# Performance work log

Hardware: AMD Instinct MI355X
Metric: run time of the kernel (lower is better)

## Reference

```python
import jax, jax.numpy as jnp
import numpy as np

NUM_HEADS = 8
GEM_P = 3.0
GEM_EPS = 1e-6
L2_EPS = 1e-12


def _l2norm(x):
    n = jnp.sqrt(jnp.sum(x * x, axis=-1, keepdims=True))
    return x / jnp.maximum(n, L2_EPS)


def setup_inputs() -> dict:
    key = jax.random.key(0)
    ks = jax.random.split(key, 7)
    B, Ci, H, W = 8, 256, 40, 40
    D, N = 128, 32768
    image_feat = jax.random.normal(ks[0], (B, Ci, H, W), dtype=jnp.float32)
    cloud_feat = jax.random.normal(ks[1], (N, D), dtype=jnp.float32)
    cloud_bids = jax.random.randint(ks[2], (N,), 0, B, dtype=jnp.int32)
    W1 = jax.random.normal(ks[3], (Ci, D), dtype=jnp.float32) * (1.0 / np.sqrt(Ci))
    b1 = jnp.zeros((D,), dtype=jnp.float32)
    W2 = jax.random.normal(ks[4], (D, Ci), dtype=jnp.float32) * (1.0 / np.sqrt(D))
    b2 = jnp.zeros((Ci,), dtype=jnp.float32)
    return {"image_feat": image_feat, "cloud_feat": cloud_feat, "cloud_bids": cloud_bids,
            "W1": W1, "b1": b1, "W2": W2, "b2": b2}


def _gem(x, axis):
    # generalized-mean pooling: (mean(clamp(x,eps)^p))^(1/p)
    xp = jnp.clip(x, GEM_EPS, None) ** GEM_P
    return jnp.mean(xp, axis=axis) ** (1.0 / GEM_P)


def reference(image_feat, cloud_feat, cloud_bids, W1, b1, W2, b2):
    B, Ci, H, W = image_feat.shape
    D = W1.shape[1]
    h, dh = NUM_HEADS, D // NUM_HEADS

    # image branch: permute -> linear -> tokens
    x = jnp.einsum('bchw,cd->bhwd', image_feat, W1) + b1          # [B,H,W,D]
    tok = _l2norm(x.reshape(B, H * W, D))                          # [B,HW,D]

    # window_size=1 SA: all image tokens of a batch share coord (b,0,0,0)
    # -> full self-attention per batch window; use_proj=False -> q=k=v=feats
    q = tok.reshape(B, H * W, h, dh)
    scores = jnp.einsum('bnhd,bmhd->bhnm', q, q) * (dh ** -0.5)    # [B,h,HW,HW]
    attn = jax.nn.softmax(scores, axis=-1)
    out = jnp.einsum('bhnm,bmhd->bnhd', attn, q).reshape(B, H, W, D)

    # cloud tokens: unique voxel coords -> singleton windows -> identity attention
    cloud_out = _l2norm(cloud_feat)                                # [N,D]

    # project image tokens back to image_dim channels
    img_out = jnp.einsum('bhwd,dc->bhwc', out, W2) + b2            # [B,H,W,Ci]
    img_out = jnp.transpose(img_out, (0, 3, 1, 2))                 # [B,Ci,H,W]

    # GeM pooling
    image_gem = _gem(img_out, axis=(2, 3))                         # [B,Ci]
    cp = jnp.clip(cloud_out, GEM_EPS, None) ** GEM_P
    seg = jax.ops.segment_sum(cp, cloud_bids, num_segments=B)      # [B,D]
    cnt = jax.ops.segment_sum(jnp.ones((cloud_out.shape[0], 1), cp.dtype),
                              cloud_bids, num_segments=B)
    cloud_gem = (seg / jnp.maximum(cnt, 1.0)) ** (1.0 / GEM_P)     # [B,D]

    return (img_out, cloud_out, image_gem, cloud_gem)
```

## Files before the change

kernel.cpp:

```cpp
#include <hip/hip_runtime.h>
#include <hip/hip_bf16.h>
#include <math.h>

#define BATCH 8
#define CI    256
#define HWSZ  1600
#define DDIM  128
#define NHEAD 8
#define DH    16
#define NPTS  32768

typedef __attribute__((ext_vector_type(4))) short s16x4;
typedef __attribute__((ext_vector_type(4))) float f32x4;

#if defined(__HIP_DEVICE_COMPILE__)
  #if __has_builtin(__builtin_amdgcn_mfma_f32_16x16x16bf16_1k)
    #define MFMA16(a, b, c) __builtin_amdgcn_mfma_f32_16x16x16bf16_1k(a, b, c, 0, 0, 0)
  #elif __has_builtin(__builtin_amdgcn_mfma_f32_16x16x16_bf16)
    #define MFMA16(a, b, c) __builtin_amdgcn_mfma_f32_16x16x16_bf16(a, b, c, 0, 0, 0)
  #else
    #error "no 16x16x16 bf16 mfma builtin on this device target"
  #endif
  #if __has_builtin(__builtin_amdgcn_exp2f)
    #define EXP2(x) __builtin_amdgcn_exp2f(x)
  #else
    #define EXP2(x) exp2f(x)
  #endif
#else
  #define MFMA16(a, b, c) (c)
  #define EXP2(x) (x)
#endif

union fragu {
  s16x4 s;
  unsigned int u[2];
  uint2 u2;
};

__device__ __forceinline__ unsigned int pk_bf2(float a, float b) {
  __hip_bfloat162 h = __float22bfloat162_rn(make_float2(a, b));
  return *(unsigned int*)&h;
}
__device__ __forceinline__ float bf2f(unsigned short u) {
  return __uint_as_float(((unsigned int)u) << 16);
}

__global__ __launch_bounds__(256) void kprep(
    const float* __restrict__ W1, const float* __restrict__ W2,
    const float* __restrict__ cf, const int* __restrict__ bids,
    unsigned short* __restrict__ W1s, unsigned short* __restrict__ W2s,
    float* __restrict__ cloud_out, float* __restrict__ gaw,
    float* __restrict__ cntw) {
  __shared__ float ga[BATCH * DDIM];
  __shared__ float gc[BATCH];
  int t = threadIdx.x;
  if (blockIdx.x < 64) {
    int e = blockIdx.x * 256 + t;
    int lane = e & 63, lm = lane & 15, qd = lane >> 4;
    if (e < 8192) {
      int ks = (e >> 6) & 15, dt = e >> 10;
      const float* p = W1 + (size_t)(ks * 16 + 4 * qd) * DDIM + dt * 16 + lm;
      float f0 = p[0], f1 = p[DDIM], f2 = p[2 * DDIM], f3 = p[3 * DDIM];
      *(uint2*)&W1s[(size_t)e * 4] = make_uint2(pk_bf2(f0, f1), pk_bf2(f2, f3));
    } else {
      int e2 = e - 8192;
      int ks = (e2 >> 6) & 7, ct = e2 >> 9;
      const float* p = W2 + (size_t)(ks * 16 + 4 * qd) * CI + ct * 16 + lm;
      float f0 = p[0], f1 = p[CI], f2 = p[2 * CI], f3 = p[3 * CI];
      *(uint2*)&W2s[(size_t)e2 * 4] = make_uint2(pk_bf2(f0, f1), pk_bf2(f2, f3));
    }
    return;
  }
  int bk = blockIdx.x - 64;
  for (int i = t; i < BATCH * DDIM; i += 256) ga[i] = 0.f;
  if (t < BATCH) gc[t] = 0.f;
  __syncthreads();
  for (int half = 0; half < 2; half++) {
    int r = bk * 128 + half * 64 + (t >> 2);
    int dq = (t & 3) * 32;
    const float* row = cf + (size_t)r * DDIM + dq;
    float4 v[8];
    float ss = 0.f;
#pragma unroll
    for (int j = 0; j < 8; j++) {
      v[j] = *(const float4*)(row + j * 4);
      ss += v[j].x*v[j].x + v[j].y*v[j].y + v[j].z*v[j].z + v[j].w*v[j].w;
    }
    ss += __shfl_xor(ss, 1);
    ss += __shfl_xor(ss, 2);
    float sc = 1.f / fmaxf(sqrtf(ss), 1e-12f);
    int bid = bids[r];
    if ((t & 3) == 0) atomicAdd(&gc[bid], 1.f);
    float* orow = cloud_out + (size_t)r * DDIM + dq;
    float* gb = &ga[bid * DDIM + dq];
#pragma unroll
    for (int j = 0; j < 8; j++) {
      float4 y;
      y.x = v[j].x * sc; y.y = v[j].y * sc; y.z = v[j].z * sc; y.w = v[j].w * sc;
      *(float4*)(orow + j * 4) = y;
      float c0 = fmaxf(y.x, 1e-6f), c1 = fmaxf(y.y, 1e-6f);
      float c2 = fmaxf(y.z, 1e-6f), c3 = fmaxf(y.w, 1e-6f);
      atomicAdd(&gb[j*4+0], c0*c0*c0);
      atomicAdd(&gb[j*4+1], c1*c1*c1);
      atomicAdd(&gb[j*4+2], c2*c2*c2);
      atomicAdd(&gb[j*4+3], c3*c3*c3);
    }
  }
  __syncthreads();
  for (int i = t; i < BATCH * DDIM; i += 256) gaw[(size_t)bk * 1024 + i] = ga[i];
  if (t < BATCH) cntw[bk * 8 + t] = gc[t];
}

__global__ __launch_bounds__(256) void k1_mfma(
    const float* __restrict__ img, const unsigned short* __restrict__ W1s,
    const float* __restrict__ b1, unsigned short* __restrict__ tokh) {
  int t = threadIdx.x, lane = t & 63, w = t >> 6;
  int lm = lane & 15, qd = lane >> 4;
  int blk = blockIdx.x;
  int b = blk / 25, n0 = (blk % 25) * 64;
  int tok = n0 + w * 16 + lm;
  const float* imgb = img + (size_t)b * CI * HWSZ;
  const s16x4* W1s4 = (const s16x4*)W1s;
  float fv[16][4];
#pragma unroll
  for (int ks = 0; ks < 16; ks++) {
    const float* p = imgb + (size_t)(ks * 16 + 4 * qd) * HWSZ + tok;
    fv[ks][0] = p[0];        fv[ks][1] = p[HWSZ];
    fv[ks][2] = p[2 * HWSZ]; fv[ks][3] = p[3 * HWSZ];
  }
  f32x4 acc[8];
#pragma unroll
  for (int dt = 0; dt < 8; dt++) acc[dt] = (f32x4){0.f, 0.f, 0.f, 0.f};
#pragma unroll
  for (int ks = 0; ks < 16; ks++) {
    fragu bf_;
    bf_.u[0] = pk_bf2(fv[ks][0], fv[ks][1]);
    bf_.u[1] = pk_bf2(fv[ks][2], fv[ks][3]);
#pragma unroll
    for (int dt = 0; dt < 8; dt++) {
      s16x4 af = W1s4[(dt * 16 + ks) * 64 + lane];
      acc[dt] = MFMA16(af, bf_.s, acc[dt]);
    }
  }
  float vals[8][4];
  float ss = 0.f;
#pragma unroll
  for (int dt = 0; dt < 8; dt++)
#pragma unroll
    for (int r = 0; r < 4; r++) {
      float v = acc[dt][r] + b1[dt * 16 + 4 * qd + r];
      vals[dt][r] = v;
      ss += v * v;
    }
  ss += __shfl_xor(ss, 16);
  ss += __shfl_xor(ss, 32);
  float inv = 1.f / fmaxf(sqrtf(ss), 1e-12f);
#pragma unroll
  for (int dt = 0; dt < 8; dt++) {
    uint2 pk = make_uint2(pk_bf2(vals[dt][0] * inv, vals[dt][1] * inv),
                          pk_bf2(vals[dt][2] * inv, vals[dt][3] * inv));
    *(uint2*)&tokh[(((size_t)b * NHEAD + dt) * HWSZ + tok) * DH + 4 * qd] = pk;
  }
}

#define NKC2     800
#define XK_STR   24
#define VT_STR   808
__global__ __launch_bounds__(512) void k2_attn(
    const unsigned short* __restrict__ tokh, float* __restrict__ numw,
    float* __restrict__ denw) {
  __shared__ unsigned short sXk[NKC2 * XK_STR];
  __shared__ unsigned short sVt[16 * VT_STR];
  const int gx = blockIdx.x;
  const int bh = gx >> 1, kc = gx & 1;
  const int t = threadIdx.x;
  const int lane = t & 63;
  const int w = t >> 6;
  const int lm = lane & 15;
  const int qd = lane >> 4;
  const unsigned short* tok = tokh + (size_t)bh * (HWSZ * DH);
  const int qw = blockIdx.y * 512 + w * 64;
  const bool active = qw < HWSZ;

  for (int r = t; r < NKC2; r += 512) {
    const uint4* src = (const uint4*)(tok + (size_t)(kc * NKC2 + r) * DH);
    union { uint4 u4[2]; unsigned short us[16]; } uu;
    uu.u4[0] = src[0]; uu.u4[1] = src[1];
    *(uint4*)&sXk[r * XK_STR]     = uu.u4[0];
    *(uint4*)&sXk[r * XK_STR + 8] = uu.u4[1];
#pragma unroll
    for (int d = 0; d < 16; d++) sVt[d * VT_STR + r] = uu.us[d];
  }

  const float SCL = 0.25f * 1.44269504088896f;
  s16x4 qf[4];
  f32x4 oacc[4];
  f32x4 dacc[4];
#pragma unroll
  for (int s = 0; s < 4; s++) {
    oacc[s] = (f32x4){0.f, 0.f, 0.f, 0.f};
    dacc[s] = (f32x4){0.f, 0.f, 0.f, 0.f};
  }
  if (active) {
#pragma unroll
    for (int s = 0; s < 4; s++) {
      const unsigned short* qs = tok + (size_t)(qw + s * 16 + lm) * DH + 4 * qd;
      s16x4 raw = *(const s16x4*)qs;
      fragu q;
      q.u[0] = pk_bf2(bf2f((unsigned short)raw[0]) * SCL,
                      bf2f((unsigned short)raw[1]) * SCL);
      q.u[1] = pk_bf2(bf2f((unsigned short)raw[2]) * SCL,
                      bf2f((unsigned short)raw[3]) * SCL);
      qf[s] = q.s;
    }
  }
  __syncthreads();

  if (active) {
    fragu ones;
    ones.u[0] = 0x3F803F80u;
    ones.u[1] = 0x3F803F80u;
#pragma unroll 2
    for (int st = 0; st < NKC2 / 16; st++) {
      int n0 = st * 16;
      s16x4 kf = *(const s16x4*)&sXk[(n0 + lm) * XK_STR + 4 * qd];
      s16x4 vf = *(const s16x4*)&sVt[lm * VT_STR + n0 + 4 * qd];
#pragma unroll
      for (int s = 0; s < 4; s++) {
        f32x4 sc = MFMA16(kf, qf[s], ((f32x4){0.f, 0.f, 0.f, 0.f}));
        float e0 = EXP2(sc.x), e1 = EXP2(sc.y), e2 = EXP2(sc.z), e3 = EXP2(sc.w);
        fragu pf;
        pf.u[0] = pk_bf2(e0, e1);
        pf.u[1] = pk_bf2(e2, e3);
        dacc[s] = MFMA16(ones.s, pf.s, dacc[s]);
        oacc[s] = MFMA16(vf, pf.s, oacc[s]);
      }
    }
  }

  if (active) {
#pragma unroll
    for (int s = 0; s < 4; s++) {
      size_t q = (size_t)qw + s * 16 + lm;
      float* np = numw + (((size_t)bh * 2 + kc) * HWSZ + q) * 16 + 4 * qd;
      *(f32x4*)np = oacc[s];
      if (qd == 0) denw[((size_t)bh * 2 + kc) * HWSZ + q] = dacc[s][0];
    }
  }
}

__global__ __launch_bounds__(256) void k3_mfma(
    const float* __restrict__ numw, const float* __restrict__ denw,
    const unsigned short* __restrict__ W2s, const float* __restrict__ b2,
    float* __restrict__ img_out) {
  int t = threadIdx.x, lane = t & 63, w = t >> 6;
  int lm = lane & 15, qd = lane >> 4;
  int blk = blockIdx.x;
  int b = blk / 25, n0 = (blk % 25) * 64;
  int tok = n0 + w * 16 + lm;
  const s16x4* W2s4 = (const s16x4*)W2s;
  f32x4 acc[16];
#pragma unroll
  for (int ct = 0; ct < 16; ct++) acc[ct] = (f32x4){0.f, 0.f, 0.f, 0.f};
#pragma unroll 2
  for (int ks = 0; ks < 8; ks++) {
    size_t bh2 = (size_t)(b * 8 + ks) * 2;
    const float* npb = numw + (bh2 * HWSZ + tok) * 16 + 4 * qd;
    f32x4 nv0 = *(const f32x4*)npb;
    f32x4 nv1 = *(const f32x4*)(npb + (size_t)HWSZ * 16);
    float d0 = denw[bh2 * HWSZ + tok];
    float d1 = denw[bh2 * HWSZ + HWSZ + tok];
    float inv = 1.f / (d0 + d1);
    fragu bf_;
    bf_.u[0] = pk_bf2((nv0.x + nv1.x) * inv, (nv0.y + nv1.y) * inv);
    bf_.u[1] = pk_bf2((nv0.z + nv1.z) * inv, (nv0.w + nv1.w) * inv);
#pragma unroll
    for (int ct = 0; ct < 16; ct++) {
      s16x4 af = W2s4[(ct * 8 + ks) * 64 + lane];
      acc[ct] = MFMA16(af, bf_.s, acc[ct]);
    }
  }
  float* ob = img_out + (size_t)b * CI * HWSZ;
#pragma unroll
  for (int ct = 0; ct < 16; ct++)
#pragma unroll
    for (int r = 0; r < 4; r++) {
      int ci = ct * 16 + 4 * qd + r;
      ob[(size_t)ci * HWSZ + tok] = acc[ct][r] + b2[ci];
    }
}

__global__ __launch_bounds__(256) void kpost(
    const float* __restrict__ img_out, const float* __restrict__ gaw,
    const float* __restrict__ cntw, float* __restrict__ image_gem,
    float* __restrict__ cloud_gem) {
  __shared__ float cs[BATCH];
  int t = threadIdx.x;
  if (blockIdx.x < 512) {
    int w = t >> 6, lane = t & 63;
    int row = blockIdx.x * 4 + w;
    const float* r = img_out + (size_t)row * HWSZ;
    float s = 0.f;
    for (int i = lane; i < HWSZ; i += 64) {
      float c = fmaxf(r[i], 1e-6f);
      s += c * c * c;
    }
    s += __shfl_xor(s, 1);  s += __shfl_xor(s, 2);  s += __shfl_xor(s, 4);
    s += __shfl_xor(s, 8);  s += __shfl_xor(s, 16); s += __shfl_xor(s, 32);
    if (lane == 0) image_gem[row] = powf(s * (1.f / (float)HWSZ), 1.f / 3.f);
  } else {
    int j = (blockIdx.x - 512) * 256 + t;
    if (t < BATCH) {
      float s = 0.f;
      for (int k = 0; k < 256; k++) s += cntw[k * 8 + t];
      cs[t] = s;
    }
    __syncthreads();
    float s = 0.f;
#pragma unroll 4
    for (int k = 0; k < 256; k++) s += gaw[(size_t)k * 1024 + j];
    int b = j >> 7;
    cloud_gem[j] = powf(s / fmaxf(cs[b], 1.f), 1.f / 3.f);
  }
}

extern "C" void kernel_launch(void* const* d_in, const int* in_sizes, int n_in,
                              void* d_out, int out_size, void* d_ws, size_t ws_size,
                              hipStream_t stream) {
  const float* image_feat = (const float*)d_in[0];
  const float* cloud_feat = (const float*)d_in[1];
  const int*   cloud_bids = (const int*)d_in[2];
  const float* W1 = (const float*)d_in[3];
  const float* b1 = (const float*)d_in[4];
  const float* W2 = (const float*)d_in[5];
  const float* b2 = (const float*)d_in[6];

  float* out = (float*)d_out;
  float* img_out   = out;
  float* cloud_out = out + 3276800;
  float* image_gem = out + 3276800 + 4194304;
  float* cloud_gem = image_gem + 2048;

  char* ws = (char*)d_ws;
  unsigned short* tokh = (unsigned short*)ws;
  float* numw = (float*)(ws + 3276800);
  float* denw = (float*)(ws + 16384000);
  unsigned short* W1s = (unsigned short*)(ws + 17203200);
  unsigned short* W2s = (unsigned short*)(ws + 17268736);
  float* gaw  = (float*)(ws + 17334272);
  float* cntw = (float*)(ws + 18382848);

  kprep<<<dim3(320), dim3(256), 0, stream>>>(W1, W2, cloud_feat, cloud_bids,
                                             W1s, W2s, cloud_out, gaw, cntw);
  k1_mfma<<<dim3(200), dim3(256), 0, stream>>>(image_feat, W1s, b1, tokh);
  k2_attn<<<dim3(128, 4), dim3(512), 0, stream>>>(tokh, numw, denw);
  k3_mfma<<<dim3(200), dim3(256), 0, stream>>>(numw, denw, W2s, b2, img_out);
  kpost<<<dim3(516), dim3(256), 0, stream>>>(img_out, gaw, cntw,
                                             image_gem, cloud_gem);
}
```

Measured before the change: 192.7 us.

## Rebalance attention work across 16 waves per block with rotated tile assignment

The attention kernel now launches 1024 threads per block instead of 512. Each wave handles one or two 16-query tiles inside a 400-query strip, instead of four tiles over 64 queries where some waves sat idle. The wave-to-tile mapping is rotated by key chunk and strip so the waves carrying two tiles land on different SIMDs, which spreads MFMA and exp work more evenly and removes the idle waves in the last strip. The trade-off is less reuse of each K/V fragment load from shared memory per wave, plus more waves competing for registers and LDS bandwidth.

```diff
diff --git a/kernel.cpp b/kernel.cpp
--- a/kernel.cpp
+++ b/kernel.cpp
@@ -166,23 +166,26 @@
 #define NKC2     800
 #define XK_STR   24
 #define VT_STR   808
-__global__ __launch_bounds__(512) void k2_attn(
+__global__ __launch_bounds__(1024, 8) void k2_attn(
     const unsigned short* __restrict__ tokh, float* __restrict__ numw,
     float* __restrict__ denw) {
   __shared__ unsigned short sXk[NKC2 * XK_STR];
   __shared__ unsigned short sVt[16 * VT_STR];
   const int gx = blockIdx.x;
   const int bh = gx >> 1, kc = gx & 1;
+  const int strip = blockIdx.y;
   const int t = threadIdx.x;
   const int lane = t & 63;
   const int w = t >> 6;
   const int lm = lane & 15;
   const int qd = lane >> 4;
   const unsigned short* tok = tokh + (size_t)bh * (HWSZ * DH);
-  const int qw = blockIdx.y * 512 + w * 64;
-  const bool active = qw < HWSZ;
-
-  for (int r = t; r < NKC2; r += 512) {
+
+  const int wpos = (w + 3 * (kc + 2 * strip)) & 15;
+  const int ti0 = wpos;
+  const bool has1 = (wpos <= 8);
+
+  for (int r = t; r < NKC2; r += 1024) {
     const uint4* src = (const uint4*)(tok + (size_t)(kc * NKC2 + r) * DH);
     union { uint4 u4[2]; unsigned short us[16]; } uu;
     uu.u4[0] = src[0]; uu.u4[1] = src[1];
@@ -193,55 +196,60 @@
   }
 
   const float SCL = 0.25f * 1.44269504088896f;
-  s16x4 qf[4];
-  f32x4 oacc[4];
-  f32x4 dacc[4];
-#pragma unroll
-  for (int s = 0; s < 4; s++) {
+  s16x4 qf[2];
+  f32x4 oacc[2], dacc[2];
+#pragma unroll
+  for (int s = 0; s < 2; s++) {
     oacc[s] = (f32x4){0.f, 0.f, 0.f, 0.f};
     dacc[s] = (f32x4){0.f, 0.f, 0.f, 0.f};
-  }
-  if (active) {
-#pragma unroll
-    for (int s = 0; s < 4; s++) {
-      const unsigned short* qs = tok + (size_t)(qw + s * 16 + lm) * DH + 4 * qd;
+    int ti = ti0 + 16 * s;
+    if (s == 0 || has1) {
+      int q = strip * 400 + ti * 16 + lm;
+      const unsigned short* qs = tok + (size_t)q * DH + 4 * qd;
       s16x4 raw = *(const s16x4*)qs;
-      fragu q;
-      q.u[0] = pk_bf2(bf2f((unsigned short)raw[0]) * SCL,
-                      bf2f((unsigned short)raw[1]) * SCL);
-      q.u[1] = pk_bf2(bf2f((unsigned short)raw[2]) * SCL,
-                      bf2f((unsigned short)raw[3]) * SCL);
-      qf[s] = q.s;
+      fragu qq;
+      qq.u[0] = pk_bf2(bf2f((unsigned short)raw[0]) * SCL,
+                       bf2f((unsigned short)raw[1]) * SCL);
+      qq.u[1] = pk_bf2(bf2f((unsigned short)raw[2]) * SCL,
+                       bf2f((unsigned short)raw[3]) * SCL);
+      qf[s] = qq.s;
     }
   }
   __syncthreads();
 
-  if (active) {
-    fragu ones;
-    ones.u[0] = 0x3F803F80u;
-    ones.u[1] = 0x3F803F80u;
+  fragu ones;
+  ones.u[0] = 0x3F803F80u;
+  ones.u[1] = 0x3F803F80u;
 #pragma unroll 2
-    for (int st = 0; st < NKC2 / 16; st++) {
-      int n0 = st * 16;
-      s16x4 kf = *(const s16x4*)&sXk[(n0 + lm) * XK_STR + 4 * qd];
-      s16x4 vf = *(const s16x4*)&sVt[lm * VT_STR + n0 + 4 * qd];
-#pragma unroll
-      for (int s = 0; s < 4; s++) {
-        f32x4 sc = MFMA16(kf, qf[s], ((f32x4){0.f, 0.f, 0.f, 0.f}));
-        float e0 = EXP2(sc.x), e1 = EXP2(sc.y), e2 = EXP2(sc.z), e3 = EXP2(sc.w);
-        fragu pf;
-        pf.u[0] = pk_bf2(e0, e1);
-        pf.u[1] = pk_bf2(e2, e3);
-        dacc[s] = MFMA16(ones.s, pf.s, dacc[s]);
-        oacc[s] = MFMA16(vf, pf.s, oacc[s]);
-      }
-    }
-  }
-
-  if (active) {
-#pragma unroll
-    for (int s = 0; s < 4; s++) {
-      size_t q = (size_t)qw + s * 16 + lm;
+  for (int st = 0; st < NKC2 / 16; st++) {
+    int n0 = st * 16;
+    s16x4 kf = *(const s16x4*)&sXk[(n0 + lm) * XK_STR + 4 * qd];
+    s16x4 vf = *(const s16x4*)&sVt[lm * VT_STR + n0 + 4 * qd];
+    {
+      f32x4 sc = MFMA16(kf, qf[0], ((f32x4){0.f, 0.f, 0.f, 0.f}));
+      float e0 = EXP2(sc.x), e1 = EXP2(sc.y), e2 = EXP2(sc.z), e3 = EXP2(sc.w);
+      fragu pf;
+      pf.u[0] = pk_bf2(e0, e1);
+      pf.u[1] = pk_bf2(e2, e3);
+      dacc[0] = MFMA16(ones.s, pf.s, dacc[0]);
+      oacc[0] = MFMA16(vf, pf.s, oacc[0]);
+    }
+    if (has1) {
+      f32x4 sc = MFMA16(kf, qf[1], ((f32x4){0.f, 0.f, 0.f, 0.f}));
+      float e0 = EXP2(sc.x), e1 = EXP2(sc.y), e2 = EXP2(sc.z), e3 = EXP2(sc.w);
+      fragu pf;
+      pf.u[0] = pk_bf2(e0, e1);
+      pf.u[1] = pk_bf2(e2, e3);
+      dacc[1] = MFMA16(ones.s, pf.s, dacc[1]);
+      oacc[1] = MFMA16(vf, pf.s, oacc[1]);
+    }
+  }
+
+#pragma unroll
+  for (int s = 0; s < 2; s++) {
+    int ti = ti0 + 16 * s;
+    if (s == 0 || has1) {
+      size_t q = (size_t)strip * 400 + ti * 16 + lm;
       float* np = numw + (((size_t)bh * 2 + kc) * HWSZ + q) * 16 + 4 * qd;
       *(f32x4*)np = oacc[s];
       if (qd == 0) denw[((size_t)bh * 2 + kc) * HWSZ + q] = dacc[s][0];
@@ -353,7 +361,7 @@
   kprep<<<dim3(320), dim3(256), 0, stream>>>(W1, W2, cloud_feat, cloud_bids,
                                              W1s, W2s, cloud_out, gaw, cntw);
   k1_mfma<<<dim3(200), dim3(256), 0, stream>>>(image_feat, W1s, b1, tokh);
-  k2_attn<<<dim3(128, 4), dim3(512), 0, stream>>>(tokh, numw, denw);
+  k2_attn<<<dim3(128, 4), dim3(1024), 0, stream>>>(tokh, numw, denw);
   k3_mfma<<<dim3(200), dim3(256), 0, stream>>>(numw, denw, W2s, b2, img_out);
   kpost<<<dim3(516), dim3(256), 0, stream>>>(img_out, gaw, cntw,
                                              image_gem, cloud_gem);
```

Measured after the change: 189.4 us. Within noise of the previous version (-1.7%).
